# Performance work log

Hardware: AMD Instinct MI355X
Metric: run time of the kernel (lower is better)

The kernel has to match this reference:

```python
import jax, jax.numpy as jnp
import numpy as np

D_MODEL = 512
N_HEADS = 4
D_HEAD = D_MODEL // N_HEADS
D_FF = 2048
N_LAYERS = 3
IN_DIM = 25
OUT_DIM = 1
PRE = 20          # pre_training_size
SCALE = 10.0      # scaling_factor
EPS = 1e-5


def setup_inputs() -> dict:
    key = jax.random.key(0)
    ks = jax.random.split(key, 20)
    B, S = 4, 2048
    def gn(k, shape, fan_in):
        return jax.random.normal(k, shape, jnp.float32) * (1.0 / np.sqrt(fan_in))
    return {
        "src": jax.random.normal(ks[0], (B, S, IN_DIM), jnp.float32),
        "emb_w": gn(ks[1], (D_MODEL, IN_DIM), IN_DIM),
        "emb_b": jnp.zeros((D_MODEL,), jnp.float32),
        "in_w": gn(ks[2], (N_LAYERS, 3 * D_MODEL, D_MODEL), D_MODEL),
        "in_b": jnp.zeros((N_LAYERS, 3 * D_MODEL), jnp.float32),
        "out_w": gn(ks[3], (N_LAYERS, D_MODEL, D_MODEL), D_MODEL),
        "out_b": jnp.zeros((N_LAYERS, D_MODEL), jnp.float32),
        "ln1_g": jnp.ones((N_LAYERS, D_MODEL), jnp.float32),
        "ln1_b": jnp.zeros((N_LAYERS, D_MODEL), jnp.float32),
        "ln2_g": jnp.ones((N_LAYERS, D_MODEL), jnp.float32),
        "ln2_b": jnp.zeros((N_LAYERS, D_MODEL), jnp.float32),
        "ff1_w": gn(ks[4], (N_LAYERS, D_FF, D_MODEL), D_MODEL),
        "ff1_b": jnp.zeros((N_LAYERS, D_FF), jnp.float32),
        "ff2_w": gn(ks[5], (N_LAYERS, D_MODEL, D_FF), D_FF),
        "ff2_b": jnp.zeros((N_LAYERS, D_MODEL), jnp.float32),
        "dec_w": gn(ks[6], (OUT_DIM, D_MODEL), D_MODEL),
        "dec_b": jnp.zeros((OUT_DIM,), jnp.float32),
    }


def _layer_norm(x, g, b):
    mu = jnp.mean(x, axis=-1, keepdims=True)
    var = jnp.var(x, axis=-1, keepdims=True)
    return (x - mu) * jax.lax.rsqrt(var + EPS) * g + b


def _pos_encoding(seq_len):
    # eval mode: start index 0, no dropout
    pos = jnp.arange(seq_len, dtype=jnp.float32)[:, None]           # [S,1]
    div = jnp.exp(jnp.arange(0, D_MODEL, 2, dtype=jnp.float32) * (-np.log(10000.0) / D_MODEL))  # [D/2]
    ang = pos * div                                                  # [S,D/2]
    return jnp.stack([jnp.sin(ang), jnp.cos(ang)], axis=-1).reshape(seq_len, D_MODEL)


def _causal_mask(seq_len):
    row = jnp.arange(seq_len)[:, None]
    col = jnp.arange(seq_len)[None, :]
    mask = jnp.where(col <= row, 0.0, -jnp.inf).astype(jnp.float32)
    # include_training_period=True: first PRE x PRE block unmasked
    return mask.at[:PRE, :PRE].set(0.0)


def reference(src, emb_w, emb_b, in_w, in_b, out_w, out_b,
              ln1_g, ln1_b, ln2_g, ln2_b, ff1_w, ff1_b, ff2_w, ff2_b,
              dec_w, dec_b):
    B, S, _ = src.shape
    x = src @ emb_w.T + emb_b                    # [B,S,D]
    x = x + _pos_encoding(S)[None]
    mask = _causal_mask(S)                       # [S,S]
    scale = 1.0 / np.sqrt(D_HEAD)
    for l in range(N_LAYERS):
        # --- self-attention (post-norm, eager bmm+softmax+bmm path) ---
        qkv = x @ in_w[l].T + in_b[l]            # [B,S,3D]
        q, k, v = jnp.split(qkv, 3, axis=-1)
        q = q.reshape(B, S, N_HEADS, D_HEAD).transpose(0, 2, 1, 3)
        k = k.reshape(B, S, N_HEADS, D_HEAD).transpose(0, 2, 1, 3)
        v = v.reshape(B, S, N_HEADS, D_HEAD).transpose(0, 2, 1, 3)
        scores = jnp.einsum('bhqd,bhkd->bhqk', q, k) * scale + mask
        attn = jax.nn.softmax(scores, axis=-1)   # [B,H,S,S] (need_weights=True path)
        o = jnp.einsum('bhqk,bhkd->bhqd', attn, v)
        o = o.transpose(0, 2, 1, 3).reshape(B, S, D_MODEL)
        o = o @ out_w[l].T + out_b[l]
        x = _layer_norm(x + o, ln1_g[l], ln1_b[l])
        # --- FFN ---
        h = jax.nn.relu(x @ ff1_w[l].T + ff1_b[l])
        h = h @ ff2_w[l].T + ff2_b[l]
        x = _layer_norm(x + h, ln2_g[l], ln2_b[l])
    out = jnp.tanh(x @ dec_w.T + dec_b) * SCALE  # [B,S,1]
    return out
```

## Files before the change

kernel.cpp:

```cpp
#include <hip/hip_runtime.h>

#define S_LEN 2048
#define DMODEL 512

typedef __attribute__((ext_vector_type(8))) short bf16x8;
typedef __attribute__((ext_vector_type(4))) float f32x4;
typedef __attribute__((ext_vector_type(4))) unsigned short u16x4;
typedef __attribute__((ext_vector_type(8))) unsigned short u16x8;
typedef __attribute__((ext_vector_type(2))) unsigned int u32x2;

__device__ __forceinline__ unsigned short f2bf(float f) {
    unsigned int u = __float_as_uint(f);
    u += 0x7fff + ((u >> 16) & 1);
    return (unsigned short)(u >> 16);
}
__device__ __forceinline__ float bf2f(unsigned short h) {
    return __uint_as_float(((unsigned int)h) << 16);
}
__device__ __forceinline__ unsigned int cvtpk(float lo, float hi) {
    unsigned int r;
    asm("v_cvt_pk_bf16_f32 %0, %1, %2" : "=v"(r) : "v"(lo), "v"(hi));
    return r;
}
__device__ __forceinline__ void gll16(const void* g, void* l) {
    __builtin_amdgcn_global_load_lds(
        (const __attribute__((address_space(1))) unsigned int*)g,
        (__attribute__((address_space(3))) unsigned int*)l, 16, 0, 0);
}

__global__ __launch_bounds__(256) void conv_all(
    const float4* __restrict__ in_w, const float4* __restrict__ out_w,
    const float4* __restrict__ ff1_w, const float4* __restrict__ ff2_w,
    u16x4* __restrict__ in_wb, u16x4* __restrict__ out_wb,
    u16x4* __restrict__ ff1_wb, u16x4* __restrict__ ff2_wb)
{
    int i = blockIdx.x * 256 + threadIdx.x;
    const float4* src; u16x4* dst; int j;
    if (i < 589824)        { src = in_w;  dst = in_wb;  j = i; }
    else if (i < 786432)   { src = out_w; dst = out_wb; j = i - 589824; }
    else if (i < 1572864)  { src = ff1_w; dst = ff1_wb; j = i - 786432; }
    else                   { src = ff2_w; dst = ff2_wb; j = i - 1572864; }
    float4 v = src[j];
    u16x4 o = { f2bf(v.x), f2bf(v.y), f2bf(v.z), f2bf(v.w) };
    dst[j] = o;
}

__global__ __launch_bounds__(256) void embed_kernel(
    const float* __restrict__ src, const float* __restrict__ ew,
    const float* __restrict__ eb, float* __restrict__ X,
    unsigned short* __restrict__ Xb)
{
    int rid = blockIdx.x;
    int s = rid & (S_LEN - 1);
    int tid = threadIdx.x;
    __shared__ float sr[25];
    if (tid < 25) sr[tid] = src[rid * 25 + tid];
    __syncthreads();
    #pragma unroll
    for (int rep = 0; rep < 2; rep++) {
        int d = tid + rep * 256;
        float a = eb[d];
        #pragma unroll
        for (int k = 0; k < 25; k++) a = fmaf(sr[k], ew[d * 25 + k], a);
        int i2 = d & ~1;
        float div = expf(-(float)i2 * (9.210340371976184f / 512.f));
        float ang = (float)s * div;
        a += (d & 1) ? cosf(ang) : sinf(ang);
        X[(size_t)rid * DMODEL + d] = a;
        Xb[(size_t)rid * DMODEL + d] = f2bf(a);
    }
}

template<int MODE, int BN>
__global__ __launch_bounds__(256) void gemm_bf16(
    const unsigned short* __restrict__ A, int lda,
    const unsigned short* __restrict__ W, int K,
    const float* __restrict__ bias,
    unsigned short* __restrict__ out, int ldc,
    unsigned short* __restrict__ out2, int nbn)
{
    constexpr int NJ = BN / 32;
    constexpr int WC = BN / 2;
    __shared__ __align__(16) unsigned short LdsBuf[2][(128 + BN) * 64];
    int tid = threadIdx.x;
    int lane = tid & 63, w = tid >> 6;
    int g = lane >> 4, c15 = lane & 15;
    int wm = w >> 1, wn = w & 1;
    int bm, bn;
    if (BN == 64) {
        int raw = blockIdx.x;
        int lid = ((raw & 7) << 6) | (raw >> 3);
        bn = lid & 7; bm = lid >> 3;
    } else {
        int raw = blockIdx.x;
        int per = gridDim.x >> 3;
        int lid = (raw & 7) * per + (raw >> 3);
        bn = lid % nbn; bm = lid / nbn;
    }

    f32x4 acc[4][NJ];
    #pragma unroll
    for (int i = 0; i < 4; i++)
        #pragma unroll
        for (int j = 0; j < NJ; j++) acc[i][j] = (f32x4){0.f, 0.f, 0.f, 0.f};

    auto stage = [&](int kk, int bi) {
        #pragma unroll
        for (int i = 0; i < 4; i++) {
            int chunk = tid + i * 256;
            int r = chunk >> 3, c = chunk & 7;
            int cs = c ^ (r & 7);
            gll16(A + (size_t)(bm * 128 + r) * lda + kk * 64 + cs * 8,
                  (void*)(LdsBuf[bi] + chunk * 8));
        }
        #pragma unroll
        for (int i = 0; i < BN / 32; i++) {
            int chunk = tid + i * 256;
            int r = chunk >> 3, c = chunk & 7;
            int cs = c ^ (r & 7);
            gll16(W + (size_t)(bn * BN + r) * K + kk * 64 + cs * 8,
                  (void*)(LdsBuf[bi] + 128 * 64 + chunk * 8));
        }
    };

    const int nk = K >> 6;
    stage(0, 0);
    int buf = 0;

    for (int kk = 0; kk < nk; kk++) {
        if (kk + 1 < nk) {
            stage(kk + 1, buf ^ 1);
            if constexpr (BN == 128) asm volatile("s_waitcnt vmcnt(8)" ::: "memory");
            else                     asm volatile("s_waitcnt vmcnt(6)" ::: "memory");
        } else {
            asm volatile("s_waitcnt vmcnt(0)" ::: "memory");
        }
        __builtin_amdgcn_s_barrier();
        bf16x8 a[4][2], b[NJ][2];
        #pragma unroll
        for (int mi = 0; mi < 4; mi++) {
            int row = wm * 64 + mi * 16 + c15;
            #pragma unroll
            for (int h = 0; h < 2; h++) {
                int ck = (h * 4 + g) ^ (row & 7);
                a[mi][h] = *(const bf16x8*)((const char*)LdsBuf[buf] + row * 128 + ck * 16);
            }
        }
        #pragma unroll
        for (int nj = 0; nj < NJ; nj++) {
            int row = wn * WC + nj * 16 + c15;
            #pragma unroll
            for (int h = 0; h < 2; h++) {
                int ck = (h * 4 + g) ^ (row & 7);
                b[nj][h] = *(const bf16x8*)((const char*)(LdsBuf[buf] + 128 * 64)
                                            + row * 128 + ck * 16);
            }
        }
        __builtin_amdgcn_s_setprio(1);
        #pragma unroll
        for (int h = 0; h < 2; h++)
            #pragma unroll
            for (int mi = 0; mi < 4; mi++)
                #pragma unroll
                for (int nj = 0; nj < NJ; nj++)
                    acc[mi][nj] = __builtin_amdgcn_mfma_f32_16x16x32_bf16(
                        a[mi][h], b[nj][h], acc[mi][nj], 0, 0, 0);
        __builtin_amdgcn_s_setprio(0);
        __builtin_amdgcn_s_barrier();
        buf ^= 1;
    }
    __syncthreads();

    unsigned short* scr = (unsigned short*)LdsBuf + (size_t)w * 4608;
    int colb0 = bn * BN + wn * WC;
    int rowb0 = bm * 128 + wm * 64;
    bool vout = (MODE == 3) && (colb0 >= 1024);
    #pragma unroll
    for (int nj = 0; nj < NJ; nj++) {
        float bv = bias[colb0 + nj * 16 + c15];
        #pragma unroll
        for (int mi = 0; mi < 4; mi++) {
            #pragma unroll
            for (int r = 0; r < 4; r++) {
                float v = acc[mi][nj][r] + bv;
                if (MODE == 2) v = fmaxf(v, 0.f);
                int rl = mi * 16 + g * 4 + r;
                int cl = nj * 16 + c15;
                if (!vout) scr[rl * 72 + cl] = f2bf(v);
                else       scr[cl * 72 + rl] = f2bf(v);
            }
        }
    }
    constexpr int NP = WC / 8;
    if (!vout) {
        #pragma unroll
        for (int p = 0; p < NP; p++) {
            int idx = p * 64 + lane;
            int row = idx / (WC / 8);
            int cc  = (idx % (WC / 8)) * 8;
            u16x8 v = *(const u16x8*)(scr + row * 72 + cc);
            *(u16x8*)(out + (size_t)(rowb0 + row) * ldc + colb0 + cc) = v;
        }
    } else {
        int cv0 = colb0 - 1024;
        int hh = cv0 >> 7, d0 = cv0 & 127;
        int bb = rowb0 >> 11, t0 = rowb0 & (S_LEN - 1);
        unsigned short* vbase = out2 + ((size_t)(bb * 4 + hh) * 128 + d0) * S_LEN + t0;
        #pragma unroll
        for (int p = 0; p < 8; p++) {
            int idx = p * 64 + lane;
            int rd = idx >> 3;
            int tc = (idx & 7) * 8;
            u16x8 v = *(const u16x8*)(scr + rd * 72 + tc);
            *(u16x8*)(vbase + (size_t)rd * S_LEN + tc) = v;
        }
    }
}

__global__ __launch_bounds__(256) void flash_attn(
    const unsigned short* __restrict__ QKb,
    const unsigned short* __restrict__ Vt,
    unsigned short* __restrict__ Ob,
    unsigned short* __restrict__ Opart,
    float* __restrict__ Mpart,
    float* __restrict__ Lpart)
{
    __shared__ __align__(16) unsigned short Ks[2][32 * 128];
    __shared__ __align__(16) unsigned short Vts[2][128 * 32];
    __shared__ __align__(16) unsigned short Plds[4][16 * 40];
    const float SCL2 = 0.12751742795f;
    static const unsigned char wtab[48] = {
        60, 125,126, 121,122,  56, 117,118, 113,114,
        52, 109,110, 105,106,  48, 101,102,  97, 98,
        44,  93, 94,  89, 90,  40,  85, 86,  81, 82,
        36,  77, 78,  73, 74,  32,  69, 70,  65, 66,
        28,  24,  20,  16,  12,   8,   4,   0
    };
    int tid = threadIdx.x;
    int lane = tid & 63, w = tid >> 6;
    int g = lane >> 4, c15 = lane & 15;
    int raw = blockIdx.x;
    int lid = (raw & 7) * 96 + (raw >> 3);
    int bh = lid / 48, idx = lid - bh * 48;
    int b = bh >> 2, h = bh & 3;
    int v = wtab[idx];
    int qb = v >> 2, ty = v & 3;
    int qbkt0, nkt, split;
    if (ty == 0) { qbkt0 = 0; nkt = 2 * qb + 2; split = -1; }
    else {
        int j = ty - 1;
        qbkt0 = j * (qb + 1);
        nkt = qb + 1;
        split = bh * 32 + (qb - 16) * 2 + j;
    }
    const int kt0 = qbkt0;

    bf16x8 q[4];
    {
        const unsigned short* qrow =
            QKb + (size_t)(b * S_LEN + qb * 64 + w * 16 + c15) * 1024 + h * 128;
        #pragma unroll
        for (int k0 = 0; k0 < 4; k0++) q[k0] = *(const bf16x8*)(qrow + k0 * 32 + g * 8);
    }
    f32x4 o[8];
    #pragma unroll
    for (int cd = 0; cd < 8; cd++) o[cd] = (f32x4){0.f, 0.f, 0.f, 0.f};
    float m = -3e38f, l = 0.f;

    auto stage = [&](int kt, int bi) {
        #pragma unroll
        for (int i = 0; i < 2; i++) {
            int chunk = tid + i * 256;
            int r = chunk >> 4, c = chunk & 15;
            int cs = (c & 8) | ((c ^ r) & 7);
            gll16(QKb + (size_t)(b * S_LEN + kt * 32 + r) * 1024 + 512 + h * 128 + cs * 8,
                  (void*)(Ks[bi] + chunk * 8));
        }
        #pragma unroll
        for (int i = 0; i < 2; i++) {
            int chunk = tid + i * 256;
            int r = chunk >> 2, c = chunk & 3;
            int cs = (c ^ r) & 3;
            gll16(Vt + ((size_t)(b * 4 + h) * 128 + r) * S_LEN + kt * 32 + cs * 8,
                  (void*)(Vts[bi] + chunk * 8));
        }
    };

    stage(kt0, 0);
    int buf = 0;

    for (int t = 0; t < nkt; t++) {
        int kt = kt0 + t;
        if (t + 1 < nkt) {
            stage(kt + 1, buf ^ 1);
            asm volatile("s_waitcnt vmcnt(4)" ::: "memory");
        } else {
            asm volatile("s_waitcnt vmcnt(0)" ::: "memory");
        }
        __builtin_amdgcn_s_barrier();
        f32x4 sf[2];
        __builtin_amdgcn_s_setprio(1);
        #pragma unroll
        for (int c = 0; c < 2; c++) {
            sf[c] = (f32x4){0.f, 0.f, 0.f, 0.f};
            int tok16 = c * 16 + c15;
            #pragma unroll
            for (int k0 = 0; k0 < 4; k0++) {
                int ck = k0 * 4 + g;
                int cs = (ck & 8) | ((ck ^ tok16) & 7);
                bf16x8 kf = *(const bf16x8*)((const char*)Ks[buf] + tok16 * 256 + cs * 16);
                sf[c] = __builtin_amdgcn_mfma_f32_16x16x32_bf16(kf, q[k0], sf[c], 0, 0, 0);
            }
        }
        __builtin_amdgcn_s_setprio(0);
        if (kt >= 2 * qb) {
            int qr = qb * 64 + w * 16 + c15;
            #pragma unroll
            for (int c = 0; c < 2; c++)
                #pragma unroll
                for (int r = 0; r < 4; r++) {
                    int tok = kt * 32 + c * 16 + g * 4 + r;
                    bool ok = (tok <= qr) || (qr < 20 && tok < 20);
                    if (!ok) sf[c][r] = -3e38f;
                }
        }
        float t0 = fmaxf(fmaxf(sf[0][0], sf[0][1]), fmaxf(sf[0][2], sf[0][3]));
        float t1 = fmaxf(fmaxf(sf[1][0], sf[1][1]), fmaxf(sf[1][2], sf[1][3]));
        float mt = fmaxf(t0, t1);
        mt = fmaxf(mt, __shfl_xor(mt, 16));
        mt = fmaxf(mt, __shfl_xor(mt, 32));
        bool need = !__all(mt <= m + 90.5f);
        float sc = 1.f;
        if (need) {
            float mn = fmaxf(m, mt);
            sc = __builtin_amdgcn_exp2f((m - mn) * SCL2);
            m = mn;
        }
        float msc2 = m * SCL2;
        #pragma unroll
        for (int c = 0; c < 2; c++)
            #pragma unroll
            for (int r = 0; r < 4; r++)
                sf[c][r] = __builtin_amdgcn_exp2f(fmaf(sf[c][r], SCL2, -msc2));
        float s0 = (sf[0][0] + sf[0][1]) + (sf[0][2] + sf[0][3]);
        float s1 = (sf[1][0] + sf[1][1]) + (sf[1][2] + sf[1][3]);
        float ls = s0 + s1;
        ls += __shfl_xor(ls, 16);
        ls += __shfl_xor(ls, 32);
        if (need) l *= sc;
        l += ls;
        #pragma unroll
        for (int c = 0; c < 2; c++) {
            u32x2 pk = { cvtpk(sf[c][0], sf[c][1]), cvtpk(sf[c][2], sf[c][3]) };
            *(u32x2*)&Plds[w][c15 * 40 + c * 16 + g * 4] = pk;
        }
        if (need) {
            float r0 = __shfl(sc, g * 4 + 0);
            float r1 = __shfl(sc, g * 4 + 1);
            float r2 = __shfl(sc, g * 4 + 2);
            float r3 = __shfl(sc, g * 4 + 3);
            #pragma unroll
            for (int cd = 0; cd < 8; cd++) {
                o[cd][0] *= r0; o[cd][1] *= r1; o[cd][2] *= r2; o[cd][3] *= r3;
            }
        }
        bf16x8 pa = *(const bf16x8*)((const char*)&Plds[w][0] + c15 * 80 + g * 16);
        __builtin_amdgcn_s_setprio(1);
        #pragma unroll
        for (int cd = 0; cd < 8; cd++) {
            int dv = cd * 16 + c15;
            int cs = (g ^ dv) & 3;
            bf16x8 vf = *(const bf16x8*)((const char*)Vts[buf] + dv * 64 + cs * 16);
            o[cd] = __builtin_amdgcn_mfma_f32_16x16x32_bf16(pa, vf, o[cd], 0, 0, 0);
        }
        __builtin_amdgcn_s_setprio(0);
        __builtin_amdgcn_s_barrier();
        buf ^= 1;
    }

    if (split < 0) {
        float li0 = 1.f / __shfl(l, g * 4 + 0);
        float li1 = 1.f / __shfl(l, g * 4 + 1);
        float li2 = 1.f / __shfl(l, g * 4 + 2);
        float li3 = 1.f / __shfl(l, g * 4 + 3);
        size_t obase = (size_t)(b * S_LEN + qb * 64 + w * 16 + g * 4) * 512 + h * 128;
        #pragma unroll
        for (int cd = 0; cd < 8; cd++) {
            Ob[obase + 0 * 512 + cd * 16 + c15] = f2bf(o[cd][0] * li0);
            Ob[obase + 1 * 512 + cd * 16 + c15] = f2bf(o[cd][1] * li1);
            Ob[obase + 2 * 512 + cd * 16 + c15] = f2bf(o[cd][2] * li2);
            Ob[obase + 3 * 512 + cd * 16 + c15] = f2bf(o[cd][3] * li3);
        }
    } else {
        unsigned short* op = Opart + (size_t)split * 8192;
        int rbo = w * 16 + g * 4;
        #pragma unroll
        for (int cd = 0; cd < 8; cd++) {
            op[(rbo + 0) * 128 + cd * 16 + c15] = f2bf(o[cd][0]);
            op[(rbo + 1) * 128 + cd * 16 + c15] = f2bf(o[cd][1]);
            op[(rbo + 2) * 128 + cd * 16 + c15] = f2bf(o[cd][2]);
            op[(rbo + 3) * 128 + cd * 16 + c15] = f2bf(o[cd][3]);
        }
        if (g == 0) {
            Mpart[split * 64 + w * 16 + c15] = m;
            Lpart[split * 64 + w * 16 + c15] = l;
        }
    }
}

__global__ __launch_bounds__(256) void attn_merge(
    const unsigned short* __restrict__ Opart,
    const float* __restrict__ Mpart, const float* __restrict__ Lpart,
    unsigned short* __restrict__ Ob)
{
    const float SCL2 = 0.12751742795f;
    int bid = blockIdx.x;
    int bh = bid >> 4, qe = bid & 15;
    int qb = 16 + qe;
    int b = bh >> 2, h = bh & 3;
    int p0 = bh * 32 + qe * 2;
    int t = threadIdx.x;
    int r = t >> 2, dq = t & 3;
    float m0 = Mpart[p0 * 64 + r], m1 = Mpart[(p0 + 1) * 64 + r];
    float l0 = Lpart[p0 * 64 + r], l1 = Lpart[(p0 + 1) * 64 + r];
    float ms = fmaxf(m0, m1);
    float w0 = __builtin_amdgcn_exp2f((m0 - ms) * SCL2);
    float w1 = __builtin_amdgcn_exp2f((m1 - ms) * SCL2);
    float linv = 1.f / (l0 * w0 + l1 * w1);
    w0 *= linv; w1 *= linv;
    const unsigned short* o0 = Opart + (size_t)p0 * 8192 + r * 128 + dq * 32;
    const unsigned short* o1 = o0 + 8192;
    unsigned short* od = Ob + (size_t)(b * S_LEN + qb * 64 + r) * 512 + h * 128 + dq * 32;
    #pragma unroll
    for (int i = 0; i < 4; i++) {
        u16x8 a = *(const u16x8*)(o0 + i * 8);
        u16x8 c = *(const u16x8*)(o1 + i * 8);
        u16x8 d;
        #pragma unroll
        for (int j = 0; j < 8; j++)
            d[j] = f2bf(bf2f(a[j]) * w0 + bf2f(c[j]) * w1);
        *(u16x8*)(od + i * 8) = d;
    }
}

__global__ __launch_bounds__(256) void add_ln_kernel(
    float* __restrict__ X, const unsigned short* __restrict__ D,
    const float* __restrict__ gw, const float* __restrict__ bw,
    unsigned short* __restrict__ Xb)
{
    int wv = threadIdx.x >> 6, lane = threadIdx.x & 63;
    int row = blockIdx.x * 4 + wv;
    size_t base = (size_t)row * DMODEL + lane * 8;
    float4 x0 = *(const float4*)(X + base);
    float4 x1 = *(const float4*)(X + base + 4);
    u16x8 d8 = *(const u16x8*)(D + base);
    float v[8];
    v[0] = x0.x + bf2f(d8[0]); v[1] = x0.y + bf2f(d8[1]);
    v[2] = x0.z + bf2f(d8[2]); v[3] = x0.w + bf2f(d8[3]);
    v[4] = x1.x + bf2f(d8[4]); v[5] = x1.y + bf2f(d8[5]);
    v[6] = x1.z + bf2f(d8[6]); v[7] = x1.w + bf2f(d8[7]);
    float s = 0.f, sq = 0.f;
    #pragma unroll
    for (int i = 0; i < 8; i++) { s += v[i]; sq = fmaf(v[i], v[i], sq); }
    #pragma unroll
    for (int off = 32; off > 0; off >>= 1) {
        s  += __shfl_xor(s, off);
        sq += __shfl_xor(sq, off);
    }
    float mu = s * (1.f / DMODEL);
    float var = sq * (1.f / DMODEL) - mu * mu;
    float rs = rsqrtf(var + 1e-5f);
    float4 g0 = *(const float4*)(gw + lane * 8);
    float4 g1 = *(const float4*)(gw + lane * 8 + 4);
    float4 b0 = *(const float4*)(bw + lane * 8);
    float4 b1 = *(const float4*)(bw + lane * 8 + 4);
    float y[8];
    y[0] = (v[0] - mu) * rs * g0.x + b0.x; y[1] = (v[1] - mu) * rs * g0.y + b0.y;
    y[2] = (v[2] - mu) * rs * g0.z + b0.z; y[3] = (v[3] - mu) * rs * g0.w + b0.w;
    y[4] = (v[4] - mu) * rs * g1.x + b1.x; y[5] = (v[5] - mu) * rs * g1.y + b1.y;
    y[6] = (v[6] - mu) * rs * g1.z + b1.z; y[7] = (v[7] - mu) * rs * g1.w + b1.w;
    float4 o0 = { y[0], y[1], y[2], y[3] };
    float4 o1 = { y[4], y[5], y[6], y[7] };
    *(float4*)(X + base) = o0;
    *(float4*)(X + base + 4) = o1;
    u16x8 ob;
    #pragma unroll
    for (int i = 0; i < 8; i++) ob[i] = f2bf(y[i]);
    *(u16x8*)(Xb + base) = ob;
}

__global__ __launch_bounds__(256) void decoder_kernel(
    const float* __restrict__ X, const float* __restrict__ w,
    const float* __restrict__ bias, float* __restrict__ out)
{
    int tid = threadIdx.x;
    int lane = tid & 63;
    int row = blockIdx.x * 4 + (tid >> 6);
    float s = 0.f;
    size_t base = (size_t)row * DMODEL;
    #pragma unroll
    for (int i = 0; i < 8; i++) s = fmaf(X[base + lane + i * 64], w[lane + i * 64], s);
    #pragma unroll
    for (int off = 32; off > 0; off >>= 1) s += __shfl_down(s, off);
    if (lane == 0) out[row] = tanhf(s + bias[0]) * 10.0f;
}

extern "C" void kernel_launch(void* const* d_in, const int* in_sizes, int n_in,
                              void* d_out, int out_size, void* d_ws, size_t ws_size,
                              hipStream_t stream)
{
    const float* src   = (const float*)d_in[0];
    const float* emb_w = (const float*)d_in[1];
    const float* emb_b = (const float*)d_in[2];
    const float* in_w  = (const float*)d_in[3];
    const float* in_b  = (const float*)d_in[4];
    const float* out_w = (const float*)d_in[5];
    const float* out_b = (const float*)d_in[6];
    const float* ln1_g = (const float*)d_in[7];
    const float* ln1_b = (const float*)d_in[8];
    const float* ln2_g = (const float*)d_in[9];
    const float* ln2_b = (const float*)d_in[10];
    const float* ff1_w = (const float*)d_in[11];
    const float* ff1_b = (const float*)d_in[12];
    const float* ff2_w = (const float*)d_in[13];
    const float* ff2_b = (const float*)d_in[14];
    const float* dec_w = (const float*)d_in[15];
    const float* dec_b = (const float*)d_in[16];

    char* ws = (char*)d_ws;
    float*          X   = (float*)ws;
    unsigned short* Xb  = (unsigned short*)(ws + (16u << 20));
    unsigned short* Pb  = (unsigned short*)(ws + (24u << 20));
    unsigned short* Ob  = (unsigned short*)(ws + (32u << 20));
    unsigned short* QKb = (unsigned short*)(ws + (40u << 20));
    unsigned short* Vt  = (unsigned short*)(ws + (56u << 20));
    unsigned short* Hb  = (unsigned short*)(ws + (40u << 20));
    unsigned short* Opart = (unsigned short*)(ws + (16u << 20));
    float* Mpart = (float*)(ws + (24u << 20));
    float* Lpart = Mpart + 512 * 64;
    unsigned short* in_wb  = (unsigned short*)(ws + (72u << 20));
    unsigned short* out_wb = in_wb  + 3u * 1536 * 512;
    unsigned short* ff1_wb = out_wb + 3u * 512 * 512;
    unsigned short* ff2_wb = ff1_wb + 3u * 2048 * 512;
    float* outp = (float*)d_out;
    const int M = 4 * S_LEN;

    conv_all<<<9216, 256, 0, stream>>>(
        (const float4*)in_w, (const float4*)out_w,
        (const float4*)ff1_w, (const float4*)ff2_w,
        (u16x4*)in_wb, (u16x4*)out_wb, (u16x4*)ff1_wb, (u16x4*)ff2_wb);

    embed_kernel<<<M, 256, 0, stream>>>(src, emb_w, emb_b, X, Xb);

    for (int l = 0; l < 3; l++) {
        gemm_bf16<3, 128><<<dim3(768), 256, 0, stream>>>(
            Xb, 512, in_wb + (size_t)l * 1536 * 512, 512, in_b + l * 1536,
            QKb, 1024, Vt, 12);
        flash_attn<<<768, 256, 0, stream>>>(QKb, Vt, Ob, Opart, Mpart, Lpart);
        attn_merge<<<256, 256, 0, stream>>>(Opart, Mpart, Lpart, Ob);
        gemm_bf16<1, 64><<<dim3(512), 256, 0, stream>>>(
            Ob, 512, out_wb + (size_t)l * 512 * 512, 512, out_b + l * 512,
            Pb, 512, nullptr, 8);
        add_ln_kernel<<<M / 4, 256, 0, stream>>>(X, Pb, ln1_g + l * 512, ln1_b + l * 512, Xb);
        gemm_bf16<2, 128><<<dim3(1024), 256, 0, stream>>>(
            Xb, 512, ff1_wb + (size_t)l * 2048 * 512, 512, ff1_b + l * 2048,
            Hb, 2048, nullptr, 16);
        gemm_bf16<1, 64><<<dim3(512), 256, 0, stream>>>(
            Hb, 2048, ff2_wb + (size_t)l * 512 * 2048, 2048, ff2_b + l * 512,
            Pb, 512, nullptr, 8);
        add_ln_kernel<<<M / 4, 256, 0, stream>>>(X, Pb, ln2_g + l * 512, ln2_b + l * 512, Xb);
    }

    decoder_kernel<<<M / 4, 256, 0, stream>>>(X, dec_w, dec_b, outp);
}
```

Measured before the change: 491.6 us.

## Process two 64-row query tiles per flash-attention block sharing K/V tiles

Each flash-attention block now handles a 128-row query tile as two 64-row halves that share every staged K/V tile, so K/V traffic into LDS is reused across twice as many queries. The work table and the split-KV scheme are rebuilt around this: long rows are split into 2 or 3 chunks, and the merge kernel now combines up to three partials. This lowers the block count and the number of K/V loads, at the cost of higher register pressure (two sets of accumulators and Q fragments) and fewer blocks to balance across CUs.

```diff
diff --git a/kernel.cpp b/kernel.cpp
--- a/kernel.cpp
+++ b/kernel.cpp
@@ -227,45 +227,50 @@
 {
     __shared__ __align__(16) unsigned short Ks[2][32 * 128];
     __shared__ __align__(16) unsigned short Vts[2][128 * 32];
-    __shared__ __align__(16) unsigned short Plds[4][16 * 40];
+    __shared__ __align__(16) unsigned short Plds[4][2][16 * 40];
     const float SCL2 = 0.12751742795f;
-    static const unsigned char wtab[48] = {
-        60, 125,126, 121,122,  56, 117,118, 113,114,
-        52, 109,110, 105,106,  48, 101,102,  97, 98,
-        44,  93, 94,  89, 90,  40,  85, 86,  81, 82,
-        36,  77, 78,  73, 74,  32,  69, 70,  65, 66,
-        28,  24,  20,  16,  12,   8,   4,   0
+    static const unsigned char wtab[32] = {
+        41, 42, 63, 61, 62, 37, 38, 57, 58, 59, 16, 54, 55, 53, 33, 34,
+        51, 49, 50, 29, 30, 45, 46, 47, 12, 25, 26, 21, 22,  8,  4,  0
     };
     int tid = threadIdx.x;
     int lane = tid & 63, w = tid >> 6;
     int g = lane >> 4, c15 = lane & 15;
     int raw = blockIdx.x;
-    int lid = (raw & 7) * 96 + (raw >> 3);
-    int bh = lid / 48, idx = lid - bh * 48;
+    int lid = (raw & 7) * 64 + (raw >> 3);
+    int bh = lid >> 5, idx = lid & 31;
     int b = bh >> 2, h = bh & 3;
     int v = wtab[idx];
-    int qb = v >> 2, ty = v & 3;
-    int qbkt0, nkt, split;
-    if (ty == 0) { qbkt0 = 0; nkt = 2 * qb + 2; split = -1; }
+    int Q = v >> 2, ty = v & 3;
+    int T = 4 * Q + 4;
+    int kt0, nkt, split;
+    if (ty == 0) { kt0 = 0; nkt = T; split = -1; }
     else {
+        int nc = (Q <= 10) ? 2 : 3;
         int j = ty - 1;
-        qbkt0 = j * (qb + 1);
-        nkt = qb + 1;
-        split = bh * 32 + (qb - 16) * 2 + j;
-    }
-    const int kt0 = qbkt0;
-
-    bf16x8 q[4];
+        kt0 = j * T / nc;
+        nkt = (j + 1) * T / nc - kt0;
+        int off = (Q <= 10) ? (Q - 5) * 2 : 12 + (Q - 11) * 3;
+        split = bh * 27 + off + j;
+    }
+
+    bf16x8 q0[4], q1[4];
     {
-        const unsigned short* qrow =
-            QKb + (size_t)(b * S_LEN + qb * 64 + w * 16 + c15) * 1024 + h * 128;
-        #pragma unroll
-        for (int k0 = 0; k0 < 4; k0++) q[k0] = *(const bf16x8*)(qrow + k0 * 32 + g * 8);
-    }
-    f32x4 o[8];
-    #pragma unroll
-    for (int cd = 0; cd < 8; cd++) o[cd] = (f32x4){0.f, 0.f, 0.f, 0.f};
-    float m = -3e38f, l = 0.f;
+        const unsigned short* qp =
+            QKb + (size_t)(b * S_LEN + Q * 128 + w * 16 + c15) * 1024 + h * 128;
+        #pragma unroll
+        for (int k0 = 0; k0 < 4; k0++) {
+            q0[k0] = *(const bf16x8*)(qp + k0 * 32 + g * 8);
+            q1[k0] = *(const bf16x8*)(qp + 64 * 1024 + k0 * 32 + g * 8);
+        }
+    }
+    f32x4 o0[8], o1[8];
+    #pragma unroll
+    for (int cd = 0; cd < 8; cd++) {
+        o0[cd] = (f32x4){0.f, 0.f, 0.f, 0.f};
+        o1[cd] = (f32x4){0.f, 0.f, 0.f, 0.f};
+    }
+    float m0 = -3e38f, l0 = 0.f, m1 = -3e38f, l1 = 0.f;
 
     auto stage = [&](int kt, int bi) {
         #pragma unroll
@@ -298,80 +303,139 @@
             asm volatile("s_waitcnt vmcnt(0)" ::: "memory");
         }
         __builtin_amdgcn_s_barrier();
-        f32x4 sf[2];
+        bool act0 = (kt < 4 * Q + 2);
+        f32x4 sf0[2], sf1[2];
         __builtin_amdgcn_s_setprio(1);
         #pragma unroll
         for (int c = 0; c < 2; c++) {
-            sf[c] = (f32x4){0.f, 0.f, 0.f, 0.f};
+            sf0[c] = (f32x4){0.f, 0.f, 0.f, 0.f};
+            sf1[c] = (f32x4){0.f, 0.f, 0.f, 0.f};
             int tok16 = c * 16 + c15;
             #pragma unroll
             for (int k0 = 0; k0 < 4; k0++) {
                 int ck = k0 * 4 + g;
                 int cs = (ck & 8) | ((ck ^ tok16) & 7);
                 bf16x8 kf = *(const bf16x8*)((const char*)Ks[buf] + tok16 * 256 + cs * 16);
-                sf[c] = __builtin_amdgcn_mfma_f32_16x16x32_bf16(kf, q[k0], sf[c], 0, 0, 0);
+                if (act0) sf0[c] = __builtin_amdgcn_mfma_f32_16x16x32_bf16(kf, q0[k0], sf0[c], 0, 0, 0);
+                sf1[c] = __builtin_amdgcn_mfma_f32_16x16x32_bf16(kf, q1[k0], sf1[c], 0, 0, 0);
             }
         }
         __builtin_amdgcn_s_setprio(0);
-        if (kt >= 2 * qb) {
-            int qr = qb * 64 + w * 16 + c15;
+        if (act0 && kt >= 4 * Q) {
+            int qr = Q * 128 + w * 16 + c15;
             #pragma unroll
             for (int c = 0; c < 2; c++)
                 #pragma unroll
                 for (int r = 0; r < 4; r++) {
                     int tok = kt * 32 + c * 16 + g * 4 + r;
                     bool ok = (tok <= qr) || (qr < 20 && tok < 20);
-                    if (!ok) sf[c][r] = -3e38f;
+                    if (!ok) sf0[c][r] = -3e38f;
                 }
         }
-        float t0 = fmaxf(fmaxf(sf[0][0], sf[0][1]), fmaxf(sf[0][2], sf[0][3]));
-        float t1 = fmaxf(fmaxf(sf[1][0], sf[1][1]), fmaxf(sf[1][2], sf[1][3]));
-        float mt = fmaxf(t0, t1);
-        mt = fmaxf(mt, __shfl_xor(mt, 16));
-        mt = fmaxf(mt, __shfl_xor(mt, 32));
-        bool need = !__all(mt <= m + 90.5f);
-        float sc = 1.f;
-        if (need) {
-            float mn = fmaxf(m, mt);
-            sc = __builtin_amdgcn_exp2f((m - mn) * SCL2);
-            m = mn;
-        }
-        float msc2 = m * SCL2;
-        #pragma unroll
-        for (int c = 0; c < 2; c++)
-            #pragma unroll
-            for (int r = 0; r < 4; r++)
-                sf[c][r] = __builtin_amdgcn_exp2f(fmaf(sf[c][r], SCL2, -msc2));
-        float s0 = (sf[0][0] + sf[0][1]) + (sf[0][2] + sf[0][3]);
-        float s1 = (sf[1][0] + sf[1][1]) + (sf[1][2] + sf[1][3]);
-        float ls = s0 + s1;
-        ls += __shfl_xor(ls, 16);
-        ls += __shfl_xor(ls, 32);
-        if (need) l *= sc;
-        l += ls;
-        #pragma unroll
-        for (int c = 0; c < 2; c++) {
-            u32x2 pk = { cvtpk(sf[c][0], sf[c][1]), cvtpk(sf[c][2], sf[c][3]) };
-            *(u32x2*)&Plds[w][c15 * 40 + c * 16 + g * 4] = pk;
-        }
-        if (need) {
-            float r0 = __shfl(sc, g * 4 + 0);
-            float r1 = __shfl(sc, g * 4 + 1);
-            float r2 = __shfl(sc, g * 4 + 2);
-            float r3 = __shfl(sc, g * 4 + 3);
+        if (kt >= 4 * Q + 2) {
+            int qr = Q * 128 + 64 + w * 16 + c15;
+            #pragma unroll
+            for (int c = 0; c < 2; c++)
+                #pragma unroll
+                for (int r = 0; r < 4; r++) {
+                    int tok = kt * 32 + c * 16 + g * 4 + r;
+                    if (tok > qr) sf1[c][r] = -3e38f;
+                }
+        }
+        float sc0 = 1.f; bool need0 = false;
+        if (act0) {
+            float t0 = fmaxf(fmaxf(sf0[0][0], sf0[0][1]), fmaxf(sf0[0][2], sf0[0][3]));
+            float t1 = fmaxf(fmaxf(sf0[1][0], sf0[1][1]), fmaxf(sf0[1][2], sf0[1][3]));
+            float mt = fmaxf(t0, t1);
+            mt = fmaxf(mt, __shfl_xor(mt, 16));
+            mt = fmaxf(mt, __shfl_xor(mt, 32));
+            need0 = !__all(mt <= m0 + 90.5f);
+            if (need0) {
+                float mn = fmaxf(m0, mt);
+                sc0 = __builtin_amdgcn_exp2f((m0 - mn) * SCL2);
+                m0 = mn;
+            }
+            float msc = m0 * SCL2;
+            #pragma unroll
+            for (int c = 0; c < 2; c++)
+                #pragma unroll
+                for (int r = 0; r < 4; r++)
+                    sf0[c][r] = __builtin_amdgcn_exp2f(fmaf(sf0[c][r], SCL2, -msc));
+            float s0 = (sf0[0][0] + sf0[0][1]) + (sf0[0][2] + sf0[0][3]);
+            float s1 = (sf0[1][0] + sf0[1][1]) + (sf0[1][2] + sf0[1][3]);
+            float ls = s0 + s1;
+            ls += __shfl_xor(ls, 16);
+            ls += __shfl_xor(ls, 32);
+            if (need0) l0 *= sc0;
+            l0 += ls;
+            #pragma unroll
+            for (int c = 0; c < 2; c++) {
+                u32x2 pk = { cvtpk(sf0[c][0], sf0[c][1]), cvtpk(sf0[c][2], sf0[c][3]) };
+                *(u32x2*)&Plds[w][0][c15 * 40 + c * 16 + g * 4] = pk;
+            }
+        }
+        {
+            float t0 = fmaxf(fmaxf(sf1[0][0], sf1[0][1]), fmaxf(sf1[0][2], sf1[0][3]));
+            float t1 = fmaxf(fmaxf(sf1[1][0], sf1[1][1]), fmaxf(sf1[1][2], sf1[1][3]));
+            float mt = fmaxf(t0, t1);
+            mt = fmaxf(mt, __shfl_xor(mt, 16));
+            mt = fmaxf(mt, __shfl_xor(mt, 32));
+            bool need1 = !__all(mt <= m1 + 90.5f);
+            float sc1 = 1.f;
+            if (need1) {
+                float mn = fmaxf(m1, mt);
+                sc1 = __builtin_amdgcn_exp2f((m1 - mn) * SCL2);
+                m1 = mn;
+            }
+            float msc = m1 * SCL2;
+            #pragma unroll
+            for (int c = 0; c < 2; c++)
+                #pragma unroll
+                for (int r = 0; r < 4; r++)
+                    sf1[c][r] = __builtin_amdgcn_exp2f(fmaf(sf1[c][r], SCL2, -msc));
+            float s0 = (sf1[0][0] + sf1[0][1]) + (sf1[0][2] + sf1[0][3]);
+            float s1 = (sf1[1][0] + sf1[1][1]) + (sf1[1][2] + sf1[1][3]);
+            float ls = s0 + s1;
+            ls += __shfl_xor(ls, 16);
+            ls += __shfl_xor(ls, 32);
+            if (need1) l1 *= sc1;
+            l1 += ls;
+            #pragma unroll
+            for (int c = 0; c < 2; c++) {
+                u32x2 pk = { cvtpk(sf1[c][0], sf1[c][1]), cvtpk(sf1[c][2], sf1[c][3]) };
+                *(u32x2*)&Plds[w][1][c15 * 40 + c * 16 + g * 4] = pk;
+            }
+            if (need1) {
+                float r0 = __shfl(sc1, g * 4 + 0);
+                float r1 = __shfl(sc1, g * 4 + 1);
+                float r2 = __shfl(sc1, g * 4 + 2);
+                float r3 = __shfl(sc1, g * 4 + 3);
+                #pragma unroll
+                for (int cd = 0; cd < 8; cd++) {
+                    o1[cd][0] *= r0; o1[cd][1] *= r1; o1[cd][2] *= r2; o1[cd][3] *= r3;
+                }
+            }
+        }
+        if (need0) {
+            float r0 = __shfl(sc0, g * 4 + 0);
+            float r1 = __shfl(sc0, g * 4 + 1);
+            float r2 = __shfl(sc0, g * 4 + 2);
+            float r3 = __shfl(sc0, g * 4 + 3);
             #pragma unroll
             for (int cd = 0; cd < 8; cd++) {
-                o[cd][0] *= r0; o[cd][1] *= r1; o[cd][2] *= r2; o[cd][3] *= r3;
-            }
-        }
-        bf16x8 pa = *(const bf16x8*)((const char*)&Plds[w][0] + c15 * 80 + g * 16);
+                o0[cd][0] *= r0; o0[cd][1] *= r1; o0[cd][2] *= r2; o0[cd][3] *= r3;
+            }
+        }
+        bf16x8 pa0 = *(const bf16x8*)((const char*)&Plds[w][0][0] + c15 * 80 + g * 16);
+        bf16x8 pa1 = *(const bf16x8*)((const char*)&Plds[w][1][0] + c15 * 80 + g * 16);
         __builtin_amdgcn_s_setprio(1);
         #pragma unroll
         for (int cd = 0; cd < 8; cd++) {
             int dv = cd * 16 + c15;
             int cs = (g ^ dv) & 3;
             bf16x8 vf = *(const bf16x8*)((const char*)Vts[buf] + dv * 64 + cs * 16);
-            o[cd] = __builtin_amdgcn_mfma_f32_16x16x32_bf16(pa, vf, o[cd], 0, 0, 0);
+            if (act0) o0[cd] = __builtin_amdgcn_mfma_f32_16x16x32_bf16(pa0, vf, o0[cd], 0, 0, 0);
+            o1[cd] = __builtin_amdgcn_mfma_f32_16x16x32_bf16(pa1, vf, o1[cd], 0, 0, 0);
         }
         __builtin_amdgcn_s_setprio(0);
         __builtin_amdgcn_s_barrier();
@@ -379,31 +443,43 @@
     }
 
     if (split < 0) {
-        float li0 = 1.f / __shfl(l, g * 4 + 0);
-        float li1 = 1.f / __shfl(l, g * 4 + 1);
-        float li2 = 1.f / __shfl(l, g * 4 + 2);
-        float li3 = 1.f / __shfl(l, g * 4 + 3);
-        size_t obase = (size_t)(b * S_LEN + qb * 64 + w * 16 + g * 4) * 512 + h * 128;
+        float li0 = 1.f / __shfl(l0, g * 4 + 0);
+        float li1 = 1.f / __shfl(l0, g * 4 + 1);
+        float li2 = 1.f / __shfl(l0, g * 4 + 2);
+        float li3 = 1.f / __shfl(l0, g * 4 + 3);
+        float lj0 = 1.f / __shfl(l1, g * 4 + 0);
+        float lj1 = 1.f / __shfl(l1, g * 4 + 1);
+        float lj2 = 1.f / __shfl(l1, g * 4 + 2);
+        float lj3 = 1.f / __shfl(l1, g * 4 + 3);
+        size_t ob0 = (size_t)(b * S_LEN + Q * 128 + w * 16 + g * 4) * 512 + h * 128;
+        size_t ob1 = ob0 + (size_t)64 * 512;
         #pragma unroll
         for (int cd = 0; cd < 8; cd++) {
-            Ob[obase + 0 * 512 + cd * 16 + c15] = f2bf(o[cd][0] * li0);
-            Ob[obase + 1 * 512 + cd * 16 + c15] = f2bf(o[cd][1] * li1);
-            Ob[obase + 2 * 512 + cd * 16 + c15] = f2bf(o[cd][2] * li2);
-            Ob[obase + 3 * 512 + cd * 16 + c15] = f2bf(o[cd][3] * li3);
+            Ob[ob0 + 0 * 512 + cd * 16 + c15] = f2bf(o0[cd][0] * li0);
+            Ob[ob0 + 1 * 512 + cd * 16 + c15] = f2bf(o0[cd][1] * li1);
+            Ob[ob0 + 2 * 512 + cd * 16 + c15] = f2bf(o0[cd][2] * li2);
+            Ob[ob0 + 3 * 512 + cd * 16 + c15] = f2bf(o0[cd][3] * li3);
+            Ob[ob1 + 0 * 512 + cd * 16 + c15] = f2bf(o1[cd][0] * lj0);
+            Ob[ob1 + 1 * 512 + cd * 16 + c15] = f2bf(o1[cd][1] * lj1);
+            Ob[ob1 + 2 * 512 + cd * 16 + c15] = f2bf(o1[cd][2] * lj2);
+            Ob[ob1 + 3 * 512 + cd * 16 + c15] = f2bf(o1[cd][3] * lj3);
         }
     } else {
-        unsigned short* op = Opart + (size_t)split * 8192;
+        unsigned short* op = Opart + (size_t)split * 16384;
         int rbo = w * 16 + g * 4;
         #pragma unroll
         for (int cd = 0; cd < 8; cd++) {
-            op[(rbo + 0) * 128 + cd * 16 + c15] = f2bf(o[cd][0]);
-            op[(rbo + 1) * 128 + cd * 16 + c15] = f2bf(o[cd][1]);
-            op[(rbo + 2) * 128 + cd * 16 + c15] = f2bf(o[cd][2]);
-            op[(rbo + 3) * 128 + cd * 16 + c15] = f2bf(o[cd][3]);
+            #pragma unroll
+            for (int r = 0; r < 4; r++) {
+                op[(rbo + r) * 128 + cd * 16 + c15]      = f2bf(o0[cd][r]);
+                op[(rbo + 64 + r) * 128 + cd * 16 + c15] = f2bf(o1[cd][r]);
+            }
         }
         if (g == 0) {
-            Mpart[split * 64 + w * 16 + c15] = m;
-            Lpart[split * 64 + w * 16 + c15] = l;
+            Mpart[split * 128 + w * 16 + c15]      = m0;
+            Mpart[split * 128 + 64 + w * 16 + c15] = m1;
+            Lpart[split * 128 + w * 16 + c15]      = l0;
+            Lpart[split * 128 + 64 + w * 16 + c15] = l1;
         }
     }
 }
@@ -415,31 +491,49 @@
 {
     const float SCL2 = 0.12751742795f;
     int bid = blockIdx.x;
-    int bh = bid >> 4, qe = bid & 15;
-    int qb = 16 + qe;
+    int bh = bid / 11, Qe = bid - bh * 11;
+    int Q = 5 + Qe;
     int b = bh >> 2, h = bh & 3;
-    int p0 = bh * 32 + qe * 2;
+    int nc = (Q <= 10) ? 2 : 3;
+    int off = (Q <= 10) ? (Q - 5) * 2 : 12 + (Q - 11) * 3;
+    int p0 = bh * 27 + off;
     int t = threadIdx.x;
-    int r = t >> 2, dq = t & 3;
-    float m0 = Mpart[p0 * 64 + r], m1 = Mpart[(p0 + 1) * 64 + r];
-    float l0 = Lpart[p0 * 64 + r], l1 = Lpart[(p0 + 1) * 64 + r];
-    float ms = fmaxf(m0, m1);
-    float w0 = __builtin_amdgcn_exp2f((m0 - ms) * SCL2);
-    float w1 = __builtin_amdgcn_exp2f((m1 - ms) * SCL2);
-    float linv = 1.f / (l0 * w0 + l1 * w1);
-    w0 *= linv; w1 *= linv;
-    const unsigned short* o0 = Opart + (size_t)p0 * 8192 + r * 128 + dq * 32;
-    const unsigned short* o1 = o0 + 8192;
-    unsigned short* od = Ob + (size_t)(b * S_LEN + qb * 64 + r) * 512 + h * 128 + dq * 32;
-    #pragma unroll
-    for (int i = 0; i < 4; i++) {
-        u16x8 a = *(const u16x8*)(o0 + i * 8);
-        u16x8 c = *(const u16x8*)(o1 + i * 8);
+    int r = t >> 1, ch = (t & 1) * 64;
+    float mi[3], li[3], wi[3];
+    #pragma unroll
+    for (int i = 0; i < 3; i++) {
+        mi[i] = (i < nc) ? Mpart[(p0 + i) * 128 + r] : -3e38f;
+        li[i] = (i < nc) ? Lpart[(p0 + i) * 128 + r] : 0.f;
+    }
+    float ms = fmaxf(fmaxf(mi[0], mi[1]), mi[2]);
+    float lsum = 0.f;
+    #pragma unroll
+    for (int i = 0; i < 3; i++) {
+        wi[i] = (i < nc) ? __builtin_amdgcn_exp2f((mi[i] - ms) * SCL2) : 0.f;
+        lsum += li[i] * wi[i];
+    }
+    float linv = 1.f / lsum;
+    #pragma unroll
+    for (int i = 0; i < 3; i++) wi[i] *= linv;
+    unsigned short* od = Ob + (size_t)(b * S_LEN + Q * 128 + r) * 512 + h * 128 + ch;
+    size_t obase = (size_t)p0 * 16384 + r * 128 + ch;
+    #pragma unroll
+    for (int k = 0; k < 8; k++) {
+        float acc[8];
+        #pragma unroll
+        for (int j = 0; j < 8; j++) acc[j] = 0.f;
+        #pragma unroll
+        for (int i = 0; i < 3; i++) {
+            if (i < nc) {
+                u16x8 a = *(const u16x8*)(Opart + obase + (size_t)i * 16384 + k * 8);
+                #pragma unroll
+                for (int j = 0; j < 8; j++) acc[j] += bf2f(a[j]) * wi[i];
+            }
+        }
         u16x8 d;
         #pragma unroll
-        for (int j = 0; j < 8; j++)
-            d[j] = f2bf(bf2f(a[j]) * w0 + bf2f(c[j]) * w1);
-        *(u16x8*)(od + i * 8) = d;
+        for (int j = 0; j < 8; j++) d[j] = f2bf(acc[j]);
+        *(u16x8*)(od + k * 8) = d;
     }
 }
 
@@ -536,8 +630,8 @@
     unsigned short* Vt  = (unsigned short*)(ws + (56u << 20));
     unsigned short* Hb  = (unsigned short*)(ws + (40u << 20));
     unsigned short* Opart = (unsigned short*)(ws + (16u << 20));
-    float* Mpart = (float*)(ws + (24u << 20));
-    float* Lpart = Mpart + 512 * 64;
+    float* Mpart = (float*)(ws + (30u << 20));
+    float* Lpart = Mpart + 432 * 128;
     unsigned short* in_wb  = (unsigned short*)(ws + (72u << 20));
     unsigned short* out_wb = in_wb  + 3u * 1536 * 512;
     unsigned short* ff1_wb = out_wb + 3u * 512 * 512;
@@ -556,8 +650,8 @@
         gemm_bf16<3, 128><<<dim3(768), 256, 0, stream>>>(
             Xb, 512, in_wb + (size_t)l * 1536 * 512, 512, in_b + l * 1536,
             QKb, 1024, Vt, 12);
-        flash_attn<<<768, 256, 0, stream>>>(QKb, Vt, Ob, Opart, Mpart, Lpart);
-        attn_merge<<<256, 256, 0, stream>>>(Opart, Mpart, Lpart, Ob);
+        flash_attn<<<512, 256, 0, stream>>>(QKb, Vt, Ob, Opart, Mpart, Lpart);
+        attn_merge<<<176, 256, 0, stream>>>(Opart, Mpart, Lpart, Ob);
         gemm_bf16<1, 64><<<dim3(512), 256, 0, stream>>>(
             Ob, 512, out_wb + (size_t)l * 512 * 512, 512, out_b + l * 512,
             Pb, 512, nullptr, 8);
```

Result: slower. 549.7 us (+11.8%).
